# Kernel tuning notes

Hardware: AMD Instinct MI355X
Metric: run time of the kernel (lower is better)

Reference implementation:

```python
import jax, jax.numpy as jnp
import numpy as np

GROUP_SIZE = 128  # infeatures // n_groups = 4096 // 32


def setup_inputs() -> dict:
    key = jax.random.key(0)
    k1, k2, k3, k4 = jax.random.split(key, 4)
    M, K, N = 256, 4096, 4096
    n_groups = K // GROUP_SIZE  # 32
    A = jax.random.normal(k1, (M, K), dtype=jnp.float32)
    # uint4 quantized weights, stored unpacked as int32 in [0, 16)
    qweight = jax.random.randint(k2, (N, K), 0, 16, dtype=jnp.int32)
    scales = jax.random.uniform(k3, (N, n_groups), dtype=jnp.float32) * 0.05 + 1e-3
    zeros = jax.random.uniform(k4, (N, n_groups), dtype=jnp.float32) * 15.0
    return {"A": A, "qweight": qweight, "scales": scales, "zeros": zeros}


def reference(A, qweight, scales, zeros):
    # Fused dequant + GEMM: W[n,k] = (q[n,k] - zeros[n, k//G]) * scales[n, k//G]
    N, K = qweight.shape
    s = jnp.repeat(scales, GROUP_SIZE, axis=1)   # [N, K]
    z = jnp.repeat(zeros, GROUP_SIZE, axis=1)    # [N, K]
    W = (qweight.astype(A.dtype) - z) * s        # dequantized weight [N, K]
    # Linear: Y = A @ W^T  -> [M, N]
    return jnp.einsum('mk,nk->mn', A, W)
```

## Files before the change

### kernel.cpp

```cpp
#include <hip/hip_runtime.h>

typedef __attribute__((ext_vector_type(8))) short bf16x8;
typedef __attribute__((ext_vector_type(4))) float f32x4;

#define MDIM 256
#define NDIM 4096
#define KDIM 4096
#define KP8 (KDIM / 8)
#define NGRP 32

typedef const __attribute__((address_space(1))) void* gas_ptr;
typedef __attribute__((address_space(3))) void* las_ptr;

__device__ __forceinline__ unsigned short f2bf(float f) {
  union { float f; unsigned int u; } v;
  v.f = f;
  unsigned int r = v.u + 0x7FFFu + ((v.u >> 16) & 1u);
  return (unsigned short)(r >> 16);
}

__device__ __forceinline__ void gl_lds16(const void* g, void* l) {
  __builtin_amdgcn_global_load_lds((gas_ptr)g, (las_ptr)l, 16, 0, 0);
}

__global__ void prep_kernel(const float* __restrict__ A, const int* __restrict__ q,
                            unsigned short* __restrict__ Ab,
                            unsigned int* __restrict__ qp) {
  int i = blockIdx.x * 256 + threadIdx.x;
  if (i < NDIM * KP8) {
    const int4* p = reinterpret_cast<const int4*>(q) + (size_t)i * 2;
    int4 a = p[0], b = p[1];
    unsigned int d = (unsigned)(a.x & 15) | ((unsigned)(a.y & 15) << 4) |
                     ((unsigned)(a.z & 15) << 8) | ((unsigned)(a.w & 15) << 12) |
                     ((unsigned)(b.x & 15) << 16) | ((unsigned)(b.y & 15) << 20) |
                     ((unsigned)(b.z & 15) << 24) | ((unsigned)(b.w & 15) << 28);
    qp[i] = d;
  } else {
    int j = i - NDIM * KP8;
    float4 v = reinterpret_cast<const float4*>(A)[j];
    ushort4 o;
    o.x = f2bf(v.x); o.y = f2bf(v.y); o.z = f2bf(v.z); o.w = f2bf(v.w);
    reinterpret_cast<ushort4*>(Ab)[j] = o;
  }
}

#define BM 256
#define BN 64
#define BK 64
#define SPLITK 4
#define KLOC (KDIM / SPLITK)
#define NTL (KLOC / BK)
#define GPS (KLOC / 128)

__global__ __launch_bounds__(512, 1) void gemm_big(
    const unsigned short* __restrict__ Ab, const unsigned int* __restrict__ qp,
    const float* __restrict__ sc, const float* __restrict__ zr,
    float* __restrict__ out) {
  __shared__ __align__(16) unsigned short A_lds[4][BM * BK];
  __shared__ __align__(16) unsigned short W_lds[2][BN * BK];
  __shared__ float s_lds[BN * GPS];
  __shared__ float zs_lds[BN * GPS];

  const int tid = threadIdx.x;
  const int lane = tid & 63;
  const int wave = tid >> 6;
  const int wm = wave >> 1;
  const int wn = wave & 1;

  const int bid = blockIdx.x;
  const int xcd = bid & 7;
  const int j = bid >> 3;
  const int ks = j >> 3;
  const int nl = j & 7;
  const int n0 = (xcd * 8 + nl) * BN;
  const int kbase = ks * KLOC;

  {
    int n = tid >> 3, g = tid & 7;
    float s = sc[(size_t)(n0 + n) * NGRP + ks * GPS + g];
    float z = zr[(size_t)(n0 + n) * NGRP + ks * GPS + g];
    s_lds[tid] = s;
    zs_lds[tid] = z * s;
  }

  const unsigned short* Abase = Ab + kbase;
  const int wrow = tid >> 3;
  const int wc = tid & 7;
  const unsigned int* qpbase = qp + (size_t)(n0 + wrow) * KP8 + (kbase >> 3) + wc;

  unsigned int qd[4];

  auto loadW = [&](int t, int idx) { qd[idx] = qpbase[t * 8]; };
  auto stageA = [&](int t, int b) {
#pragma unroll
    for (int i = 0; i < 4; ++i) {
      int cid = i * 512 + tid;
      int row = cid >> 3;
      int cp = cid & 7;
      int cs = cp ^ (row & 7);
      const unsigned short* g = Abase + (size_t)row * KDIM + t * BK + cs * 8;
      gl_lds16(g, &A_lds[b][(i * 512 + wave * 64) * 8]);
    }
  };
  auto writeW = [&](int t, int b, int idx) {
    int gg = t >> 1;
    float s = s_lds[wrow * GPS + gg];
    float zs = zs_lds[wrow * GPS + gg];
    unsigned int d = qd[idx];
    bf16x8 w;
#pragma unroll
    for (int jj = 0; jj < 8; ++jj)
      w[jj] = (short)f2bf(fmaf((float)((d >> (4 * jj)) & 15u), s, -zs));
    *reinterpret_cast<bf16x8*>(
        &W_lds[b][wrow * BK + ((wc ^ (wrow & 7)) << 3)]) = w;
  };

  f32x4 acc[4][2];
#pragma unroll
  for (int i = 0; i < 4; ++i)
#pragma unroll
    for (int n = 0; n < 2; ++n) acc[i][n] = (f32x4){0.f, 0.f, 0.f, 0.f};

  const int l15 = lane & 15;
  const int lhi = lane >> 4;
  const int ar0 = wm * 64 + l15;
  const int asw = ar0 & 7;

  auto compute = [&](int ab, int wb) {
#pragma unroll
    for (int kss = 0; kss < 2; ++kss) {
#pragma unroll
      for (int ni = 0; ni < 2; ++ni) {
        const int br = wn * 32 + ni * 16 + l15;
        bf16x8 bfr = *reinterpret_cast<const bf16x8*>(
            &W_lds[wb][br * BK + ((((kss << 2) + lhi) ^ (br & 7)) << 3)]);
#pragma unroll
        for (int mi = 0; mi < 4; ++mi) {
          bf16x8 afr = *reinterpret_cast<const bf16x8*>(
              &A_lds[ab][(ar0 + mi * 16) * BK +
                         ((((kss << 2) + lhi) ^ asw) << 3)]);
          acc[mi][ni] = __builtin_amdgcn_mfma_f32_16x16x32_bf16(
              afr, bfr, acc[mi][ni], 0, 0, 0);
        }
      }
    }
  };

  loadW(0, 0); stageA(0, 0);
  loadW(1, 1); stageA(1, 1);
  loadW(2, 2); stageA(2, 2);

  asm volatile("s_waitcnt lgkmcnt(0)" ::: "memory");
  __builtin_amdgcn_s_barrier();
  __builtin_amdgcn_sched_barrier(0);
  writeW(0, 0, 0);
  asm volatile("s_waitcnt vmcnt(10) lgkmcnt(0)" ::: "memory");
  __builtin_amdgcn_s_barrier();
  __builtin_amdgcn_sched_barrier(0);

  for (int tb = 0; tb < NTL; tb += 4) {
#pragma unroll
    for (int u = 0; u < 4; ++u) {
      const int t = tb + u;
      const int tp = (t + 3 < NTL) ? (t + 3) : 0;
      loadW(tp, (u + 3) & 3);
      stageA(tp, (u + 3) & 3);
      compute(u, u & 1);
      if (t + 1 < NTL) writeW(t + 1, (u + 1) & 1, (u + 1) & 3);
      asm volatile("s_waitcnt vmcnt(10) lgkmcnt(0)" ::: "memory");
      __builtin_amdgcn_s_barrier();
      __builtin_amdgcn_sched_barrier(0);
    }
  }

  const int col = n0 + wn * 32 + l15;
  const int rb = wm * 64 + (lhi << 2);
#pragma unroll
  for (int mi = 0; mi < 4; ++mi)
#pragma unroll
    for (int ni = 0; ni < 2; ++ni)
#pragma unroll
      for (int jj = 0; jj < 4; ++jj)
        unsafeAtomicAdd(&out[(size_t)(rb + mi * 16 + jj) * NDIM + col + ni * 16],
                        acc[mi][ni][jj]);
}

#define FBM 128
#define FBN 32
#define FSPLITK 2
#define FKLOC (KDIM / FSPLITK)
#define FNTL (FKLOC / BK)

__global__ void convA_kernel(const float* __restrict__ A,
                             unsigned short* __restrict__ Ab) {
  int i = blockIdx.x * 256 + threadIdx.x;
  float4 v = reinterpret_cast<const float4*>(A)[i];
  ushort4 o;
  o.x = f2bf(v.x); o.y = f2bf(v.y); o.z = f2bf(v.z); o.w = f2bf(v.w);
  reinterpret_cast<ushort4*>(Ab)[i] = o;
}

__global__ __launch_bounds__(256, 2) void gemm_r3(
    const unsigned short* __restrict__ Ab, const int* __restrict__ qw,
    const float* __restrict__ sc, const float* __restrict__ zr,
    float* __restrict__ out) {
  __shared__ __align__(16) unsigned short A_lds[4][FBM * BK];
  __shared__ __align__(16) unsigned short W_lds[2][FBN * BK];
  __shared__ float s_lds[FBN * 16];
  __shared__ float zs_lds[FBN * 16];

  const int tid = threadIdx.x;
  const int lane = tid & 63;
  const int wave = tid >> 6;
  const int wm = wave >> 1;
  const int wn = wave & 1;

  const int bid = blockIdx.x;
  const int x = bid & 7;
  const int j = bid >> 3;
  const int r = x * 16 + (j >> 2);
  const int c = j & 3;
  const int m0 = (c & 1) * FBM;
  const int ks = c >> 1;
  const int n0 = r * FBN;

  for (int i = tid; i < FBN * 16; i += 256) {
    int n = i >> 4;
    int g16 = i & 15;
    float s = sc[(size_t)(n0 + n) * NGRP + ks * 16 + g16];
    float z = zr[(size_t)(n0 + n) * NGRP + ks * 16 + g16];
    s_lds[i] = s;
    zs_lds[i] = z * s;
  }

  const unsigned short* Abase = Ab + (size_t)m0 * KDIM + ks * FKLOC;
  const int wrow = tid >> 3;
  const int wc = tid & 7;
  const int* qbase = qw + (size_t)(n0 + wrow) * KDIM + ks * FKLOC + wc * 8;

  int4 qr[4][2];

  auto loadW = [&](int t, int idx) {
    const int* p = qbase + t * BK;
    qr[idx][0] = *reinterpret_cast<const int4*>(p);
    qr[idx][1] = *reinterpret_cast<const int4*>(p + 4);
  };
  auto stageA = [&](int t, int b) {
#pragma unroll
    for (int i = 0; i < 4; ++i) {
      int cid = i * 256 + tid;
      int row = cid >> 3;
      int cp = cid & 7;
      int cs = cp ^ (row & 7);
      const unsigned short* g = Abase + (size_t)row * KDIM + t * BK + cs * 8;
      gl_lds16(g, &A_lds[b][(i * 256 + wave * 64) * 8]);
    }
  };
  auto writeW = [&](int t, int b, int idx) {
    int gg = t >> 1;
    float s = s_lds[wrow * 16 + gg];
    float zs = zs_lds[wrow * 16 + gg];
    int q[8] = {qr[idx][0].x, qr[idx][0].y, qr[idx][0].z, qr[idx][0].w,
                qr[idx][1].x, qr[idx][1].y, qr[idx][1].z, qr[idx][1].w};
    bf16x8 w;
#pragma unroll
    for (int jj = 0; jj < 8; ++jj)
      w[jj] = (short)f2bf(fmaf((float)q[jj], s, -zs));
    *reinterpret_cast<bf16x8*>(
        &W_lds[b][wrow * BK + ((wc ^ (wrow & 7)) << 3)]) = w;
  };

  f32x4 acc[4];
#pragma unroll
  for (int i = 0; i < 4; ++i) acc[i] = (f32x4){0.f, 0.f, 0.f, 0.f};

  const int l15 = lane & 15;
  const int lhi = lane >> 4;
  const int ar0 = wm * 64 + l15;
  const int asw = ar0 & 7;
  const int br = wn * 16 + l15;
  const int bsw = br & 7;

  auto compute = [&](int ab, int wb) {
#pragma unroll
    for (int kss = 0; kss < 2; ++kss) {
      bf16x8 bfr = *reinterpret_cast<const bf16x8*>(
          &W_lds[wb][br * BK + ((((kss << 2) + lhi) ^ bsw) << 3)]);
#pragma unroll
      for (int mi = 0; mi < 4; ++mi) {
        bf16x8 afr = *reinterpret_cast<const bf16x8*>(
            &A_lds[ab][(ar0 + mi * 16) * BK + ((((kss << 2) + lhi) ^ asw) << 3)]);
        acc[mi] = __builtin_amdgcn_mfma_f32_16x16x32_bf16(afr, bfr, acc[mi], 0, 0, 0);
      }
    }
  };

  loadW(0, 0); stageA(0, 0);
  loadW(1, 1); stageA(1, 1);
  loadW(2, 2); stageA(2, 2);

  asm volatile("s_waitcnt lgkmcnt(0)" ::: "memory");
  __builtin_amdgcn_s_barrier();
  __builtin_amdgcn_sched_barrier(0);
  writeW(0, 0, 0);
  asm volatile("s_waitcnt vmcnt(12) lgkmcnt(0)" ::: "memory");
  __builtin_amdgcn_s_barrier();
  __builtin_amdgcn_sched_barrier(0);

  for (int tb = 0; tb < FNTL; tb += 4) {
#pragma unroll
    for (int u = 0; u < 4; ++u) {
      const int t = tb + u;
      const int tp = (t + 3 < FNTL) ? (t + 3) : 0;
      loadW(tp, (u + 3) & 3);
      stageA(tp, (u + 3) & 3);
      compute(u, u & 1);
      if (t + 1 < FNTL) writeW(t + 1, (u + 1) & 1, (u + 1) & 3);
      asm volatile("s_waitcnt vmcnt(12) lgkmcnt(0)" ::: "memory");
      __builtin_amdgcn_s_barrier();
      __builtin_amdgcn_sched_barrier(0);
    }
  }

  const int col = n0 + wn * 16 + l15;
  const int rb = m0 + wm * 64 + (lhi << 2);
#pragma unroll
  for (int mi = 0; mi < 4; ++mi)
#pragma unroll
    for (int jj = 0; jj < 4; ++jj)
      unsafeAtomicAdd(&out[(size_t)(rb + mi * 16 + jj) * NDIM + col],
                      acc[mi][jj]);
}

extern "C" void kernel_launch(void* const* d_in, const int* in_sizes, int n_in,
                              void* d_out, int out_size, void* d_ws, size_t ws_size,
                              hipStream_t stream) {
  const float* A = (const float*)d_in[0];
  const int* qw = (const int*)d_in[1];
  const float* sc = (const float*)d_in[2];
  const float* zr = (const float*)d_in[3];
  float* out = (float*)d_out;

  hipMemsetAsync(d_out, 0, (size_t)MDIM * NDIM * sizeof(float), stream);

  if (ws_size >= (10u << 20)) {
    unsigned short* Ab = (unsigned short*)d_ws;
    unsigned int* qp = (unsigned int*)((char*)d_ws + (2u << 20));
    prep_kernel<<<9216, 256, 0, stream>>>(A, qw, Ab, qp);
    gemm_big<<<(NDIM / BN) * SPLITK, 512, 0, stream>>>(Ab, qp, sc, zr, out);
  } else {
    unsigned short* Ab = (unsigned short*)d_ws;
    convA_kernel<<<(MDIM * KDIM / 4) / 256, 256, 0, stream>>>(A, Ab);
    gemm_r3<<<(MDIM / FBM) * (NDIM / FBN) * FSPLITK, 256, 0, stream>>>(
        Ab, qw, sc, zr, out);
  }
}
```

Before: 129.6 us.

## Retile dequant GEMM to 64x128 blocks with 256 threads and fuse output zeroing

The main GEMM changes from 256x64 tiles with 512 threads and one block per CU to 64x128 tiles with 256 threads and two blocks per CU. It also splits M across blocks, giving 512 blocks instead of 256. Each thread now loads 16 bytes of packed weights at once and dequantizes 32 values, and a new block-to-XCD mapping covers the M and K splits. The separate hipMemsetAsync of the output is folded into the prep kernel as an extra segment, removing one launch. In exchange, the A tile is re-read by more blocks and there are more atomic adds, while occupancy and latency hiding should improve.

```diff
diff --git a/kernel.cpp b/kernel.cpp
--- a/kernel.cpp
+++ b/kernel.cpp
@@ -23,11 +23,15 @@
   __builtin_amdgcn_global_load_lds((gas_ptr)g, (las_ptr)l, 16, 0, 0);
 }
 
+#define SEG0 (NDIM * KP8)
+#define SEG1 (SEG0 + MDIM * KDIM / 4)
+#define SEG2 (SEG1 + MDIM * NDIM / 4)
 __global__ void prep_kernel(const float* __restrict__ A, const int* __restrict__ q,
                             unsigned short* __restrict__ Ab,
-                            unsigned int* __restrict__ qp) {
+                            unsigned int* __restrict__ qp,
+                            float* __restrict__ out) {
   int i = blockIdx.x * 256 + threadIdx.x;
-  if (i < NDIM * KP8) {
+  if (i < SEG0) {
     const int4* p = reinterpret_cast<const int4*>(q) + (size_t)i * 2;
     int4 a = p[0], b = p[1];
     unsigned int d = (unsigned)(a.x & 15) | ((unsigned)(a.y & 15) << 4) |
@@ -35,24 +39,27 @@
                      ((unsigned)(b.x & 15) << 16) | ((unsigned)(b.y & 15) << 20) |
                      ((unsigned)(b.z & 15) << 24) | ((unsigned)(b.w & 15) << 28);
     qp[i] = d;
-  } else {
-    int j = i - NDIM * KP8;
+  } else if (i < SEG1) {
+    int j = i - SEG0;
     float4 v = reinterpret_cast<const float4*>(A)[j];
     ushort4 o;
     o.x = f2bf(v.x); o.y = f2bf(v.y); o.z = f2bf(v.z); o.w = f2bf(v.w);
     reinterpret_cast<ushort4*>(Ab)[j] = o;
-  }
-}
-
-#define BM 256
-#define BN 64
+  } else {
+    int j = i - SEG1;
+    reinterpret_cast<float4*>(out)[j] = make_float4(0.f, 0.f, 0.f, 0.f);
+  }
+}
+
+#define BM 64
+#define BN 128
 #define BK 64
 #define SPLITK 4
 #define KLOC (KDIM / SPLITK)
 #define NTL (KLOC / BK)
 #define GPS (KLOC / 128)
 
-__global__ __launch_bounds__(512, 1) void gemm_big(
+__global__ __launch_bounds__(256, 2) void gemm_v10(
     const unsigned short* __restrict__ Ab, const unsigned int* __restrict__ qp,
     const float* __restrict__ sc, const float* __restrict__ zr,
     float* __restrict__ out) {
@@ -70,78 +77,92 @@
   const int bid = blockIdx.x;
   const int xcd = bid & 7;
   const int j = bid >> 3;
-  const int ks = j >> 3;
-  const int nl = j & 7;
-  const int n0 = (xcd * 8 + nl) * BN;
+  const int sl = j >> 5;
+  const int nl = j & 31;
+  const int sid = xcd * 2 + sl;
+  const int m0 = (sid & 3) * BM;
+  const int ks = sid >> 2;
+  const int n0 = nl * BN;
   const int kbase = ks * KLOC;
 
-  {
-    int n = tid >> 3, g = tid & 7;
+  for (int i = tid; i < BN * GPS; i += 256) {
+    int n = i >> 3;
+    int g = i & 7;
     float s = sc[(size_t)(n0 + n) * NGRP + ks * GPS + g];
     float z = zr[(size_t)(n0 + n) * NGRP + ks * GPS + g];
-    s_lds[tid] = s;
-    zs_lds[tid] = z * s;
-  }
-
-  const unsigned short* Abase = Ab + kbase;
-  const int wrow = tid >> 3;
-  const int wc = tid & 7;
-  const unsigned int* qpbase = qp + (size_t)(n0 + wrow) * KP8 + (kbase >> 3) + wc;
-
-  unsigned int qd[4];
-
-  auto loadW = [&](int t, int idx) { qd[idx] = qpbase[t * 8]; };
+    s_lds[i] = s;
+    zs_lds[i] = z * s;
+  }
+  asm volatile("s_waitcnt vmcnt(0) lgkmcnt(0)" ::: "memory");
+  __builtin_amdgcn_sched_barrier(0);
+
+  const unsigned short* Abase = Ab + (size_t)m0 * KDIM + kbase;
+  const int wrow = tid >> 1;
+  const int wc = tid & 1;
+  const int4* qpbase = reinterpret_cast<const int4*>(
+      qp + (size_t)(n0 + wrow) * KP8 + (kbase >> 3)) + wc;
+
+  int4 qr[4];
+
+  auto loadW = [&](int t, int idx) { qr[idx] = qpbase[t * 2]; };
   auto stageA = [&](int t, int b) {
 #pragma unroll
-    for (int i = 0; i < 4; ++i) {
-      int cid = i * 512 + tid;
+    for (int i = 0; i < 2; ++i) {
+      int cid = i * 256 + tid;
       int row = cid >> 3;
       int cp = cid & 7;
       int cs = cp ^ (row & 7);
       const unsigned short* g = Abase + (size_t)row * KDIM + t * BK + cs * 8;
-      gl_lds16(g, &A_lds[b][(i * 512 + wave * 64) * 8]);
+      gl_lds16(g, &A_lds[b][(i * 256 + wave * 64) * 8]);
     }
   };
   auto writeW = [&](int t, int b, int idx) {
     int gg = t >> 1;
     float s = s_lds[wrow * GPS + gg];
     float zs = zs_lds[wrow * GPS + gg];
-    unsigned int d = qd[idx];
-    bf16x8 w;
-#pragma unroll
-    for (int jj = 0; jj < 8; ++jj)
-      w[jj] = (short)f2bf(fmaf((float)((d >> (4 * jj)) & 15u), s, -zs));
-    *reinterpret_cast<bf16x8*>(
-        &W_lds[b][wrow * BK + ((wc ^ (wrow & 7)) << 3)]) = w;
-  };
-
-  f32x4 acc[4][2];
-#pragma unroll
-  for (int i = 0; i < 4; ++i)
-#pragma unroll
-    for (int n = 0; n < 2; ++n) acc[i][n] = (f32x4){0.f, 0.f, 0.f, 0.f};
+    unsigned int dw[4] = {(unsigned)qr[idx].x, (unsigned)qr[idx].y,
+                          (unsigned)qr[idx].z, (unsigned)qr[idx].w};
+#pragma unroll
+    for (int c = 0; c < 4; ++c) {
+      unsigned int d = dw[c];
+      bf16x8 w;
+#pragma unroll
+      for (int e = 0; e < 8; ++e)
+        w[e] = (short)f2bf(fmaf((float)((d >> (4 * e)) & 15u), s, -zs));
+      *reinterpret_cast<bf16x8*>(
+          &W_lds[b][wrow * BK + (((wc * 4 + c) ^ (wrow & 7)) << 3)]) = w;
+    }
+  };
+
+  f32x4 acc[2][4];
+#pragma unroll
+  for (int i = 0; i < 2; ++i)
+#pragma unroll
+    for (int n = 0; n < 4; ++n) acc[i][n] = (f32x4){0.f, 0.f, 0.f, 0.f};
 
   const int l15 = lane & 15;
   const int lhi = lane >> 4;
-  const int ar0 = wm * 64 + l15;
+  const int ar0 = wm * 32 + l15;
   const int asw = ar0 & 7;
+  const int bsw = l15 & 7;
 
   auto compute = [&](int ab, int wb) {
 #pragma unroll
     for (int kss = 0; kss < 2; ++kss) {
-#pragma unroll
-      for (int ni = 0; ni < 2; ++ni) {
-        const int br = wn * 32 + ni * 16 + l15;
+      bf16x8 afr[2];
+#pragma unroll
+      for (int mi = 0; mi < 2; ++mi)
+        afr[mi] = *reinterpret_cast<const bf16x8*>(
+            &A_lds[ab][(ar0 + mi * 16) * BK + ((((kss << 2) + lhi) ^ asw) << 3)]);
+#pragma unroll
+      for (int ni = 0; ni < 4; ++ni) {
+        const int br = wn * 64 + ni * 16 + l15;
         bf16x8 bfr = *reinterpret_cast<const bf16x8*>(
-            &W_lds[wb][br * BK + ((((kss << 2) + lhi) ^ (br & 7)) << 3)]);
-#pragma unroll
-        for (int mi = 0; mi < 4; ++mi) {
-          bf16x8 afr = *reinterpret_cast<const bf16x8*>(
-              &A_lds[ab][(ar0 + mi * 16) * BK +
-                         ((((kss << 2) + lhi) ^ asw) << 3)]);
+            &W_lds[wb][br * BK + ((((kss << 2) + lhi) ^ bsw) << 3)]);
+#pragma unroll
+        for (int mi = 0; mi < 2; ++mi)
           acc[mi][ni] = __builtin_amdgcn_mfma_f32_16x16x32_bf16(
-              afr, bfr, acc[mi][ni], 0, 0, 0);
-        }
+              afr[mi], bfr, acc[mi][ni], 0, 0, 0);
       }
     }
   };
@@ -150,11 +171,10 @@
   loadW(1, 1); stageA(1, 1);
   loadW(2, 2); stageA(2, 2);
 
-  asm volatile("s_waitcnt lgkmcnt(0)" ::: "memory");
   __builtin_amdgcn_s_barrier();
   __builtin_amdgcn_sched_barrier(0);
   writeW(0, 0, 0);
-  asm volatile("s_waitcnt vmcnt(10) lgkmcnt(0)" ::: "memory");
+  asm volatile("s_waitcnt vmcnt(6) lgkmcnt(0)" ::: "memory");
   __builtin_amdgcn_s_barrier();
   __builtin_amdgcn_sched_barrier(0);
 
@@ -165,20 +185,20 @@
       const int tp = (t + 3 < NTL) ? (t + 3) : 0;
       loadW(tp, (u + 3) & 3);
       stageA(tp, (u + 3) & 3);
-      compute(u, u & 1);
+      compute(u & 3, u & 1);
       if (t + 1 < NTL) writeW(t + 1, (u + 1) & 1, (u + 1) & 3);
-      asm volatile("s_waitcnt vmcnt(10) lgkmcnt(0)" ::: "memory");
+      asm volatile("s_waitcnt vmcnt(6) lgkmcnt(0)" ::: "memory");
       __builtin_amdgcn_s_barrier();
       __builtin_amdgcn_sched_barrier(0);
     }
   }
 
-  const int col = n0 + wn * 32 + l15;
-  const int rb = wm * 64 + (lhi << 2);
-#pragma unroll
-  for (int mi = 0; mi < 4; ++mi)
-#pragma unroll
-    for (int ni = 0; ni < 2; ++ni)
+  const int col = n0 + wn * 64 + l15;
+  const int rb = m0 + wm * 32 + (lhi << 2);
+#pragma unroll
+  for (int mi = 0; mi < 2; ++mi)
+#pragma unroll
+    for (int ni = 0; ni < 4; ++ni)
 #pragma unroll
       for (int jj = 0; jj < 4; ++jj)
         unsafeAtomicAdd(&out[(size_t)(rb + mi * 16 + jj) * NDIM + col + ni * 16],
@@ -341,14 +361,14 @@
   const float* zr = (const float*)d_in[3];
   float* out = (float*)d_out;
 
-  hipMemsetAsync(d_out, 0, (size_t)MDIM * NDIM * sizeof(float), stream);
-
   if (ws_size >= (10u << 20)) {
     unsigned short* Ab = (unsigned short*)d_ws;
     unsigned int* qp = (unsigned int*)((char*)d_ws + (2u << 20));
-    prep_kernel<<<9216, 256, 0, stream>>>(A, qw, Ab, qp);
-    gemm_big<<<(NDIM / BN) * SPLITK, 512, 0, stream>>>(Ab, qp, sc, zr, out);
+    prep_kernel<<<10240, 256, 0, stream>>>(A, qw, Ab, qp, out);
+    gemm_v10<<<(MDIM / BM) * (NDIM / BN) * SPLITK, 256, 0, stream>>>(
+        Ab, qp, sc, zr, out);
   } else {
+    hipMemsetAsync(d_out, 0, (size_t)MDIM * NDIM * sizeof(float), stream);
     unsigned short* Ab = (unsigned short*)d_ws;
     convA_kernel<<<(MDIM * KDIM / 4) / 256, 256, 0, stream>>>(A, Ab);
     gemm_r3<<<(MDIM / FBM) * (NDIM / FBN) * FSPLITK, 256, 0, stream>>>(
```

New measurement: 134.5 us. 3.8% more time.
